# Performance work log

Measured on AMD Instinct MI355X. Metric: run time of the kernel, lower is better.

Reference implementation:

```python
import jax, jax.numpy as jnp
import numpy as np

PAD_IDX = 0
B, T, S, H, V = 64, 32, 64, 1024, 32000


def setup_inputs() -> dict:
    key = jax.random.key(0)
    ks = jax.random.split(key, 12)
    s = 0.02
    emb_tbl = jax.random.normal(ks[0], (V, H), jnp.float32) * s
    emb_tbl = emb_tbl.at[PAD_IDX].set(0.0)  # padding_idx row is zero
    return {
        "input": jax.random.randint(ks[1], (B, T), 0, V),
        "memory": jax.random.normal(ks[2], (1, B, H), jnp.float32),
        "encoder_output": jax.random.normal(ks[3], (B, S, H), jnp.float32),
        "xs_len": jax.random.randint(ks[4], (B,), 1, S + 1),
        "embedding": emb_tbl,
        "w_ih": jax.random.normal(ks[5], (3 * H, 2 * H), jnp.float32) * s,
        "w_hh": jax.random.normal(ks[6], (3 * H, H), jnp.float32) * s,
        "b_ih": jnp.zeros((3 * H,), jnp.float32),
        "b_hh": jnp.zeros((3 * H,), jnp.float32),
        "l1": jax.random.normal(ks[7], (H, H), jnp.float32) * s,
        "l2": jax.random.normal(ks[8], (H, 2 * H), jnp.float32) * s,
        "w_out": jax.random.normal(ks[9], (V, H), jnp.float32) * s,
        "b_out": jnp.zeros((V,), jnp.float32),
    }


def _gru_cell(x, h, w_ih, w_hh, b_ih, b_hh):
    # torch.nn.GRUCell math
    gi = x @ w_ih.T + b_ih          # [B, 3H]
    gh = h @ w_hh.T + b_hh          # [B, 3H]
    ir, iz, inn = jnp.split(gi, 3, axis=1)
    hr, hz, hn = jnp.split(gh, 3, axis=1)
    r = jax.nn.sigmoid(ir + hr)
    z = jax.nn.sigmoid(iz + hz)
    n = jnp.tanh(inn + r * hn)
    return (1.0 - z) * n + z * h


def _attention(hidden, enc, seq_mask, l1, l2):
    # hidden: [B,H], enc: [B,S,H], seq_mask: [B,S] float {0,1}
    q = hidden @ l1.T                              # [B,H]
    score = jnp.einsum("bsh,bh->bs", enc, q)       # [B,S]
    masked = seq_mask * score
    # faithful to `masked_att[masked_att == 0] = -1e10`
    masked = jnp.where(masked == 0.0, -1e10, masked)
    attn = jax.nn.softmax(masked, axis=1)          # softmax over source positions
    ctx = jnp.einsum("bs,bsh->bh", attn, enc)      # [B,H]
    out = jnp.tanh(jnp.concatenate([ctx, hidden], axis=1) @ l2.T)
    return out, attn


def reference(input, memory, encoder_output, xs_len, embedding,
              w_ih, w_hh, b_ih, b_hh, l1, l2, w_out, b_out):
    emb = embedding[input]                         # [B,T,H]
    emb_t = jnp.swapaxes(emb, 0, 1)                # [T,B,H]
    h0 = memory[0]                                 # [B,H]
    ctx0 = jnp.zeros_like(h0)
    s_len = encoder_output.shape[1]
    seq_mask = (jnp.arange(s_len)[None, :] < xs_len[:, None]).astype(emb.dtype)  # [B,S]

    def step(carry, e_t):
        h_prev, ctx = carry
        x = jnp.concatenate([e_t, ctx], axis=1)    # [B,2H]
        h = _gru_cell(x, h_prev, w_ih, w_hh, b_ih, b_hh)
        ctx_new, attn = _attention(h, encoder_output, seq_mask, l1, l2)
        scores = jax.nn.log_softmax(ctx_new @ w_out.T + b_out, axis=1)  # [B,V]
        return (h, ctx_new), (scores, attn)

    (h_fin, ctx_fin), (all_scores, all_attn) = jax.lax.scan(step, (h0, ctx0), emb_t)
    decoder_output = jnp.swapaxes(all_scores, 0, 1)        # [B,T,V]
    decoder_hidden = h_fin[None, :, :]                     # [1,B,H]
    attention_weights = jnp.swapaxes(all_attn, 0, 1)       # [B,T,S]
    return decoder_output, decoder_hidden, attention_weights, ctx_fin
```

## Files before the change

kernel.cpp:

```cpp
#include <hip/hip_runtime.h>


#define B_ 64
#define T_ 32
#define S_ 64
#define H_ 1024
#define V_ 32000
#define NB_ 256
#define LDS_BYTES 152064

#define HID_OFF 65536000L
#define ATT_OFF 65601536L
#define CTF_OFF 65732608L

typedef __attribute__((ext_vector_type(8))) short bf16x8;
typedef __attribute__((ext_vector_type(4))) float f32x4;
typedef __attribute__((ext_vector_type(4))) unsigned int u32x4;
typedef unsigned short u16;
typedef unsigned long long u64;

__device__ __forceinline__ u16 f2bf(float v) {
  unsigned int u = __float_as_uint(v);
  unsigned int r = (u + 0x7fffu + ((u >> 16) & 1u)) >> 16;
  return (u16)r;
}
__device__ __forceinline__ float bf2f(u16 h) {
  return __uint_as_float(((unsigned int)h) << 16);
}
__device__ __forceinline__ void split2(float v, u16* hi, u16* lo) {
  u16 h = f2bf(v);
  *hi = h;
  *lo = f2bf(v - bf2f(h));
}

__device__ __forceinline__ u64 aload_u64(const void* p) {
  return __hip_atomic_load((const u64*)p, __ATOMIC_RELAXED, __HIP_MEMORY_SCOPE_AGENT);
}
__device__ __forceinline__ unsigned aload_u32(const void* p) {
  return __hip_atomic_load((const unsigned*)p, __ATOMIC_RELAXED, __HIP_MEMORY_SCOPE_AGENT);
}
__device__ __forceinline__ void astore_u64(void* p, u64 v) {
  __hip_atomic_store((u64*)p, v, __ATOMIC_RELAXED, __HIP_MEMORY_SCOPE_AGENT);
}
__device__ __forceinline__ void astore_f32(float* p, float v) {
  __hip_atomic_store((unsigned*)p, __float_as_uint(v), __ATOMIC_RELAXED,
                     __HIP_MEMORY_SCOPE_AGENT);
}


__global__ void k_split(const float* __restrict__ src, u16* __restrict__ hi,
                        u16* __restrict__ lo, int n) {
  int i = blockIdx.x * blockDim.x + threadIdx.x;
  int stride = gridDim.x * blockDim.x;
  for (; i < n; i += stride) split2(src[i], &hi[i], &lo[i]);
}

__global__ void k_tobf(const float* __restrict__ src, u16* __restrict__ dst, int n) {
  int i = blockIdx.x * blockDim.x + threadIdx.x;
  int stride = gridDim.x * blockDim.x;
  for (; i < n; i += stride) dst[i] = f2bf(src[i]);
}

__global__ void k_l1t(const float* __restrict__ l1, u16* __restrict__ hi,
                      u16* __restrict__ lo) {
  __shared__ float tile[64][65];
  int it = blockIdx.x & 15, kt = blockIdx.x >> 4;
  for (int q = 0; q < 16; ++q) {
    int idx = q * 256 + threadIdx.x;
    int r = idx >> 6, c = idx & 63;
    tile[r][c] = l1[(long)(it * 64 + r) * H_ + kt * 64 + c];
  }
  __syncthreads();
  for (int q = 0; q < 16; ++q) {
    int idx = q * 256 + threadIdx.x;
    int r = idx >> 6, c = idx & 63;
    long o = (long)(kt * 64 + r) * H_ + it * 64 + c;
    split2(tile[c][r], &hi[o], &lo[o]);
  }
}

__global__ void k_embx(const int* __restrict__ inp, const float* __restrict__ emb,
                       u16* __restrict__ hi, u16* __restrict__ lo) {
  int bt = blockIdx.x;
  int b = bt >> 5, t = bt & 31;
  int id = inp[b * T_ + t];
  const float* src = emb + (long)id * H_;
  long base = (long)(t * B_ + b) * H_;
  for (int k = threadIdx.x; k < H_; k += 256) split2(src[k], &hi[base + k], &lo[base + k]);
}

__global__ void k_h0(const float* __restrict__ mem, u16* __restrict__ hh,
                     u16* __restrict__ hl) {
  int i = blockIdx.x * 256 + threadIdx.x;
  float v = mem[i];
  split2(v, &hh[i], &hl[i]);
}

__global__ void k_guard(float* out, float v) {
  if (blockIdx.x == 0 && threadIdx.x == 0) out[0] = v;
}

template <int SPLIT, int OMODE>
__launch_bounds__(256)
__global__ void k_gemm128(const u16* __restrict__ Ah, const u16* __restrict__ Al,
                          const u16* __restrict__ Bh, const u16* __restrict__ Bl,
                          float* __restrict__ C, const float* __restrict__ bias,
                          int Mtiles, int Ntiles, int K, int Arow, int Brow, int Crow) {
  (void)Ntiles;
  int bx = blockIdx.x;
  int mt = bx % Mtiles, nt = bx / Mtiles;
  int m0 = mt * 128, n0 = nt * 128;

  __shared__ __attribute__((aligned(16))) u16 lds[(SPLIT ? 4 : 2) * 4096];
  char* L = (char*)lds;
  const int tid = threadIdx.x;
  const int lane = tid & 63, wid = tid >> 6;
  const int wm = wid & 1, wn = wid >> 1;
  const int l15 = lane & 15, kq = lane >> 4;

  f32x4 acc[4][4];
  const f32x4 z4 = {0.f, 0.f, 0.f, 0.f};
#pragma unroll
  for (int i = 0; i < 4; ++i)
#pragma unroll
    for (int j = 0; j < 4; ++j) acc[i][j] = z4;

  const int ksteps = K >> 5;
  for (int kt = 0; kt < ksteps; ++kt) {
    __syncthreads();
#pragma unroll
    for (int h2 = 0; h2 < 2; ++h2) {
      int r = (tid >> 2) + (h2 << 6);
      int slot = tid & 3;
      int so = ((slot ^ (r & 3)) << 4);
      long ga = (long)(m0 + r) * Arow + (kt << 5) + (slot << 3);
      long gb = (long)(n0 + r) * Brow + (kt << 5) + (slot << 3);
      *(u32x4*)(L + r * 64 + so) = *(const u32x4*)(Ah + ga);
      *(u32x4*)(L + 8192 + r * 64 + so) = *(const u32x4*)(Bh + gb);
      if (SPLIT) {
        *(u32x4*)(L + 16384 + r * 64 + so) = *(const u32x4*)(Al + ga);
        *(u32x4*)(L + 24576 + r * 64 + so) = *(const u32x4*)(Bl + gb);
      }
    }
    __syncthreads();
    bf16x8 aH[4], bH[4], aL[4], bL[4];
#pragma unroll
    for (int mi = 0; mi < 4; ++mi) {
      int r = (wm << 6) + (mi << 4) + l15;
      int off = r * 64 + ((kq ^ (r & 3)) << 4);
      aH[mi] = *(const bf16x8*)(L + off);
      if (SPLIT) aL[mi] = *(const bf16x8*)(L + 16384 + off);
    }
#pragma unroll
    for (int ni = 0; ni < 4; ++ni) {
      int c = (wn << 6) + (ni << 4) + l15;
      int off = c * 64 + ((kq ^ (c & 3)) << 4);
      bH[ni] = *(const bf16x8*)(L + 8192 + off);
      if (SPLIT) bL[ni] = *(const bf16x8*)(L + 24576 + off);
    }
#pragma unroll
    for (int mi = 0; mi < 4; ++mi)
#pragma unroll
      for (int ni = 0; ni < 4; ++ni) {
        acc[mi][ni] = __builtin_amdgcn_mfma_f32_16x16x32_bf16(aH[mi], bH[ni], acc[mi][ni], 0, 0, 0);
        if (SPLIT) {
          acc[mi][ni] = __builtin_amdgcn_mfma_f32_16x16x32_bf16(aL[mi], bH[ni], acc[mi][ni], 0, 0, 0);
          acc[mi][ni] = __builtin_amdgcn_mfma_f32_16x16x32_bf16(aH[mi], bL[ni], acc[mi][ni], 0, 0, 0);
        }
      }
  }
#pragma unroll
  for (int mi = 0; mi < 4; ++mi)
#pragma unroll
    for (int ni = 0; ni < 4; ++ni)
#pragma unroll
      for (int e = 0; e < 4; ++e) {
        int r = (wm << 6) + (mi << 4) + (kq << 2) + e;
        int c = (wn << 6) + (ni << 4) + l15;
        int gm = m0 + r, gn = n0 + c;
        float v = acc[mi][ni][e];
        if (OMODE == 0) {
          C[(long)gm * Crow + gn] = v;
        } else {
          v += bias[gn];
          C[((long)(gm & 63) * T_ + (gm >> 6)) * V_ + gn] = v;
        }
      }
}

__device__ __forceinline__ void gridbar(unsigned* flags, unsigned seq) {
  __syncthreads();
  if (threadIdx.x == 0)
    __hip_atomic_store(flags + blockIdx.x * 16, seq, __ATOMIC_RELEASE,
                       __HIP_MEMORY_SCOPE_AGENT);
  if (threadIdx.x < 64) {
    int l = threadIdx.x;
    for (;;) {
      unsigned a = __hip_atomic_load(flags + l * 16, __ATOMIC_RELAXED, __HIP_MEMORY_SCOPE_AGENT);
      unsigned b = __hip_atomic_load(flags + (l + 64) * 16, __ATOMIC_RELAXED, __HIP_MEMORY_SCOPE_AGENT);
      unsigned c = __hip_atomic_load(flags + (l + 128) * 16, __ATOMIC_RELAXED, __HIP_MEMORY_SCOPE_AGENT);
      unsigned d = __hip_atomic_load(flags + (l + 192) * 16, __ATOMIC_RELAXED, __HIP_MEMORY_SCOPE_AGENT);
      if (__all((a >= seq) & (b >= seq) & (c >= seq) & (d >= seq))) break;
      __builtin_amdgcn_s_sleep(1);
    }
  }
  __syncthreads();
}

__launch_bounds__(256)
__global__ void k_rec(const float* __restrict__ embi,
                      u16* __restrict__ dctx_h, u16* __restrict__ dctx_l,
                      u16* __restrict__ hh_r, u16* __restrict__ hl_r,
                      const float* __restrict__ memory,
                      const u16* __restrict__ wih_h, const u16* __restrict__ wih_l,
                      const u16* __restrict__ whh_h, const u16* __restrict__ whh_l,
                      const u16* __restrict__ l2_h, const u16* __restrict__ l2_l,
                      float* __restrict__ gip, float* __restrict__ ghp,
                      float* __restrict__ psc, float* __restrict__ ctxp,
                      const float* __restrict__ encT, const float* __restrict__ encL,
                      const int* __restrict__ xs_len,
                      const float* __restrict__ bih, const float* __restrict__ bhh,
                      float* __restrict__ dout, unsigned* flags) {
  extern __shared__ __attribute__((aligned(16))) char L[];
  char* W_HI = L;
  char* W_LO = L + 65536;
  char* A_HI = L + 131072;
  char* A_LO = L + 139264;
  float* hq = (float*)(L + 147456);
  float* at_s = (float*)(L + 148480);
  const int bx = blockIdx.x;
  const int tid = threadIdx.x;
  const int lane = tid & 63, wid = tid >> 6;
  const int wm = wid & 1, wn = wid >> 1;
  const int l15 = lane & 15, kq = lane >> 4;
  const f32x4 z4 = {0.f, 0.f, 0.f, 0.f};
  unsigned seq = 1;

  const int isGI = (bx < 96);
  const int isGH = (bx >= 96 && bx < 192);
  const int isL2 = (bx >= 192 && bx < 224);
  const int sb = bx >> 2;
  const int sq = bx & 3;
  int nt = 0, kc = 0, n0 = 0;
  const u16 *Wg_h = nullptr, *Wg_l = nullptr;
  int wrs = 0;
  if (isGI) {
    nt = bx % 48; kc = bx / 48;
    Wg_h = wih_h + 1024 + (long)nt * 64 * 2048 + kc * 512;
    Wg_l = wih_l + 1024 + (long)nt * 64 * 2048 + kc * 512;
    wrs = 2048;
  } else if (isGH) {
    int j2 = bx - 96;
    nt = j2 % 48; kc = j2 / 48;
    Wg_h = whh_h + (long)nt * 64 * 1024 + kc * 512;
    Wg_l = whh_l + (long)nt * 64 * 1024 + kc * 512;
    wrs = 1024;
  } else if (isL2) {
    n0 = (bx - 192) << 5;
    Wg_h = l2_h + 1024 + (long)n0 * 2048;
    Wg_l = l2_l + 1024 + (long)n0 * 2048;
    wrs = 2048;
  }

  if (isGI || isGH) {
    for (int e = tid; e < 4096; e += 256) {
      int st = e >> 8, r = (e >> 2) & 63, slot = e & 3;
      long g = (long)r * wrs + st * 32 + slot * 8;
      int o = st * 4096 + r * 64 + ((slot ^ (r & 3)) << 4);
      *(u32x4*)(W_HI + o) = *(const u32x4*)(Wg_h + g);
      *(u32x4*)(W_LO + o) = *(const u32x4*)(Wg_l + g);
    }
  } else if (isL2) {
    for (int e = tid; e < 4096; e += 256) {
      int st = e >> 7, r = (e >> 2) & 31, slot = e & 3;
      long g = (long)r * wrs + st * 32 + slot * 8;
      int o = st * 2048 + r * 64 + ((slot ^ (r & 3)) << 4);
      *(u32x4*)(W_HI + o) = *(const u32x4*)(Wg_h + g);
      *(u32x4*)(W_LO + o) = *(const u32x4*)(Wg_l + g);
    }
  }
  __syncthreads();

  float hpv = memory[sb * 1024 + sq * 256 + tid];

  const int pr = tid >> 2, ps = tid & 3;
  const int ao = pr * 64 + ((ps ^ (pr & 3)) << 4);

  for (int t = 0; t < T_; ++t) {
    if (isGI || isGH) {
      const u16* Ah;
      const u16* Al;
      float* outp;
      if (isGI) {
        Ah = dctx_h + (long)t * 65536 + kc * 512;
        Al = dctx_l + (long)t * 65536 + kc * 512;
        outp = gip + (long)kc * 196608 + nt * 64;
      } else {
        Ah = hh_r + (long)t * 65536 + kc * 512;
        Al = hl_r + (long)t * 65536 + kc * 512;
        outp = ghp + (long)kc * 196608 + nt * 64;
      }
      const long g0 = (long)pr * 1024 + ps * 8;
      u32x4 ph0 = *(const u32x4*)(Ah + g0);
      u32x4 ph1 = *(const u32x4*)(Ah + g0 + 32);
      u32x4 pl0 = *(const u32x4*)(Al + g0);
      u32x4 pl1 = *(const u32x4*)(Al + g0 + 32);

      f32x4 acc[2][2];
#pragma unroll
      for (int i = 0; i < 2; ++i)
#pragma unroll
        for (int j = 0; j < 2; ++j) acc[i][j] = z4;

      for (int kt = 0; kt < 8; ++kt) {
        __syncthreads();
        *(u32x4*)(A_HI + ao) = ph0;
        *(u32x4*)(A_HI + 4096 + ao) = ph1;
        *(u32x4*)(A_LO + ao) = pl0;
        *(u32x4*)(A_LO + 4096 + ao) = pl1;
        __syncthreads();
        if (kt < 7) {
          long g = g0 + (kt + 1) * 64;
          ph0 = *(const u32x4*)(Ah + g);
          ph1 = *(const u32x4*)(Ah + g + 32);
          pl0 = *(const u32x4*)(Al + g);
          pl1 = *(const u32x4*)(Al + g + 32);
        }
#pragma unroll
        for (int sub = 0; sub < 2; ++sub) {
          const int stw = (kt * 2 + sub) * 4096;
          const int sta = sub * 4096;
          bf16x8 aH[2], aL[2], bH[2], bL[2];
#pragma unroll
          for (int mi = 0; mi < 2; ++mi) {
            int rr = (wm << 5) + (mi << 4) + l15;
            int off = rr * 64 + ((kq ^ (rr & 3)) << 4);
            aH[mi] = *(const bf16x8*)(A_HI + sta + off);
            aL[mi] = *(const bf16x8*)(A_LO + sta + off);
          }
#pragma unroll
          for (int ni = 0; ni < 2; ++ni) {
            int c = (wn << 5) + (ni << 4) + l15;
            int off = c * 64 + ((kq ^ (c & 3)) << 4);
            bH[ni] = *(const bf16x8*)(W_HI + stw + off);
            bL[ni] = *(const bf16x8*)(W_LO + stw + off);
          }
#pragma unroll
          for (int mi = 0; mi < 2; ++mi)
#pragma unroll
            for (int ni = 0; ni < 2; ++ni) {
              acc[mi][ni] = __builtin_amdgcn_mfma_f32_16x16x32_bf16(aH[mi], bH[ni], acc[mi][ni], 0, 0, 0);
              acc[mi][ni] = __builtin_amdgcn_mfma_f32_16x16x32_bf16(aL[mi], bH[ni], acc[mi][ni], 0, 0, 0);
              acc[mi][ni] = __builtin_amdgcn_mfma_f32_16x16x32_bf16(aH[mi], bL[ni], acc[mi][ni], 0, 0, 0);
            }
        }
      }
#pragma unroll
      for (int mi = 0; mi < 2; ++mi)
#pragma unroll
        for (int ni = 0; ni < 2; ++ni)
#pragma unroll
          for (int e = 0; e < 4; ++e) {
            int r = (wm << 5) + (mi << 4) + (kq << 2) + e;
            int c = (wn << 5) + (ni << 4) + l15;
            astore_f32(outp + (long)r * 3072 + c, acc[mi][ni][e]);
          }
    }
    gridbar(flags, seq++);

    {
      const int b = sb, q = sq;
      const int j = (q << 8) + tid;
      const float* eb = embi + ((long)t * 64 + b) * 3072;
      float g0r = __uint_as_float(aload_u32(gip + b * 3072 + j));
      float g1r = __uint_as_float(aload_u32(gip + 196608 + b * 3072 + j));
      float g0z = __uint_as_float(aload_u32(gip + b * 3072 + 1024 + j));
      float g1z = __uint_as_float(aload_u32(gip + 196608 + b * 3072 + 1024 + j));
      float g0n = __uint_as_float(aload_u32(gip + b * 3072 + 2048 + j));
      float g1n = __uint_as_float(aload_u32(gip + 196608 + b * 3072 + 2048 + j));
      float h0r = __uint_as_float(aload_u32(ghp + b * 3072 + j));
      float h1r = __uint_as_float(aload_u32(ghp + 196608 + b * 3072 + j));
      float h0z = __uint_as_float(aload_u32(ghp + b * 3072 + 1024 + j));
      float h1z = __uint_as_float(aload_u32(ghp + 196608 + b * 3072 + 1024 + j));
      float h0n = __uint_as_float(aload_u32(ghp + b * 3072 + 2048 + j));
      float h1n = __uint_as_float(aload_u32(ghp + 196608 + b * 3072 + 2048 + j));
      float ir = eb[j] + g0r + g1r + bih[j];
      float iz = eb[1024 + j] + g0z + g1z + bih[1024 + j];
      float in2 = eb[2048 + j] + g0n + g1n + bih[2048 + j];
      float hr = h0r + h1r + bhh[j];
      float hz = h0z + h1z + bhh[1024 + j];
      float hn = h0n + h1n + bhh[2048 + j];
      float r = 1.f / (1.f + expf(-(ir + hr)));
      float z = 1.f / (1.f + expf(-(iz + hz)));
      float n = tanhf(in2 + r * hn);
      float h = (1.f - z) * n + z * hpv;
      hpv = h;
      hq[tid] = h;
      if (t == T_ - 1) dout[HID_OFF + (long)b * 1024 + j] = h;
      __syncthreads();
      if (tid < 64) {
        u64 ph = 0, pl = 0;
#pragma unroll
        for (int ii = 0; ii < 4; ++ii) {
          u16 hi, lo;
          split2(hq[tid * 4 + ii], &hi, &lo);
          ph |= (u64)hi << (16 * ii);
          pl |= (u64)lo << (16 * ii);
        }
        long o = (long)(t + 1) * 65536 + (long)b * 1024 + (q << 8) + tid * 4;
        astore_u64(hh_r + o, ph);
        astore_u64(hl_r + o, pl);
      }
      {
        int s = tid >> 2, part = tid & 3;
        const float4* ep = (const float4*)(encT + (((long)b * 64 + s) << 10) + (q << 8) + (part << 6));
        const float4* hp = (const float4*)(hq + (part << 6));
        float dot = 0.f;
#pragma unroll
        for (int kk = 0; kk < 16; ++kk) {
          float4 e = ep[kk], a = hp[kk];
          dot += e.x * a.x + e.y * a.y + e.z * a.z + e.w * a.w;
        }
        dot += __shfl_xor(dot, 1);
        dot += __shfl_xor(dot, 2);
        if (part == 0) astore_f32(psc + (((b << 2) + q) << 6) + s, dot);
      }
    }
    gridbar(flags, seq++);

    {
      const int b = sb, q = sq;
      if (tid < 64) {
        int s = tid;
        float v = 0.f;
#pragma unroll
        for (int qq = 0; qq < 4; ++qq)
          v += __uint_as_float(aload_u32(psc + (((b << 2) + qq) << 6) + s));
        int len = xs_len[b];
        if (s >= len || v == 0.0f) v = -1e10f;
        float m = v;
#pragma unroll
        for (int off = 32; off; off >>= 1) m = fmaxf(m, __shfl_xor(m, off));
        float p = expf(v - m);
        float sum = p;
#pragma unroll
        for (int off = 32; off; off >>= 1) sum += __shfl_xor(sum, off);
        float a = p / sum;
        at_s[s] = a;
        if (q == 0) dout[ATT_OFF + ((long)b * T_ + t) * S_ + s] = a;
      }
      __syncthreads();
      {
        const float* lp = encL + (((long)b * 64 + (q << 4)) << 10) + tid * 4;
        float c0 = 0.f, c1 = 0.f, c2 = 0.f, c3 = 0.f;
#pragma unroll
        for (int s2 = 0; s2 < 16; ++s2) {
          float a = at_s[(q << 4) + s2];
          float4 e = *(const float4*)(lp + (s2 << 10));
          c0 += a * e.x; c1 += a * e.y; c2 += a * e.z; c3 += a * e.w;
        }
        u64 w0 = ((u64)__float_as_uint(c1) << 32) | __float_as_uint(c0);
        u64 w1 = ((u64)__float_as_uint(c3) << 32) | __float_as_uint(c2);
        long o = (((long)(b << 2) + q) << 10) + tid * 4;
        astore_u64(ctxp + o, w0);
        astore_u64(ctxp + o + 2, w1);
      }
    }
    gridbar(flags, seq++);

    if (isL2) {
      const u16* Ah = hh_r + (long)(t + 1) * 65536;
      const u16* Al = hl_r + (long)(t + 1) * 65536;
      const long g0 = (long)pr * 1024 + ps * 8;
      u32x4 ph0 = *(const u32x4*)(Ah + g0);
      u32x4 ph1 = *(const u32x4*)(Ah + g0 + 32);
      u32x4 pl0 = *(const u32x4*)(Al + g0);
      u32x4 pl1 = *(const u32x4*)(Al + g0 + 32);

      f32x4 acc[2];
      acc[0] = z4; acc[1] = z4;
      for (int kt = 0; kt < 16; ++kt) {
        __syncthreads();
        *(u32x4*)(A_HI + ao) = ph0;
        *(u32x4*)(A_HI + 4096 + ao) = ph1;
        *(u32x4*)(A_LO + ao) = pl0;
        *(u32x4*)(A_LO + 4096 + ao) = pl1;
        __syncthreads();
        if (kt < 15) {
          long g = g0 + (kt + 1) * 64;
          ph0 = *(const u32x4*)(Ah + g);
          ph1 = *(const u32x4*)(Ah + g + 32);
          pl0 = *(const u32x4*)(Al + g);
          pl1 = *(const u32x4*)(Al + g + 32);
        }
#pragma unroll
        for (int sub = 0; sub < 2; ++sub) {
          const int stw = (kt * 2 + sub) * 2048;
          const int sta = sub * 4096;
          bf16x8 aH[2], aL[2], bH, bL;
#pragma unroll
          for (int mi = 0; mi < 2; ++mi) {
            int rr = (wm << 5) + (mi << 4) + l15;
            int off = rr * 64 + ((kq ^ (rr & 3)) << 4);
            aH[mi] = *(const bf16x8*)(A_HI + sta + off);
            aL[mi] = *(const bf16x8*)(A_LO + sta + off);
          }
          {
            int c = (wn << 4) + l15;
            int off = c * 64 + ((kq ^ (c & 3)) << 4);
            bH = *(const bf16x8*)(W_HI + stw + off);
            bL = *(const bf16x8*)(W_LO + stw + off);
          }
#pragma unroll
          for (int mi = 0; mi < 2; ++mi) {
            acc[mi] = __builtin_amdgcn_mfma_f32_16x16x32_bf16(aH[mi], bH, acc[mi], 0, 0, 0);
            acc[mi] = __builtin_amdgcn_mfma_f32_16x16x32_bf16(aL[mi], bH, acc[mi], 0, 0, 0);
            acc[mi] = __builtin_amdgcn_mfma_f32_16x16x32_bf16(aH[mi], bL, acc[mi], 0, 0, 0);
          }
        }
      }
      __syncthreads();
      float* cf = (float*)(L + 131072);
#pragma unroll
      for (int mi = 0; mi < 2; ++mi)
#pragma unroll
        for (int e = 0; e < 4; ++e) {
          int rr = (wm << 5) + (mi << 4) + (kq << 2) + e;
          int cc = (wn << 4) + l15;
          float a = 0.f;
#pragma unroll
          for (int qq = 0; qq < 4; ++qq)
            a += __uint_as_float(aload_u32(ctxp + (((long)(rr << 2) + qq) << 10) + n0 + cc));
          float v = tanhf(acc[mi][e] + a);
          if (t == T_ - 1) dout[CTF_OFF + (long)rr * 1024 + n0 + cc] = v;
          cf[rr * 32 + cc] = v;
        }
      __syncthreads();
#pragma unroll
      for (int qq2 = 0; qq2 < 2; ++qq2) {
        int g = tid + qq2 * 256;
        int b = g >> 3, colg = g & 7;
        u64 ph = 0, pl = 0;
#pragma unroll
        for (int ii = 0; ii < 4; ++ii) {
          float v = cf[b * 32 + colg * 4 + ii];
          u16 hi, lo;
          split2(v, &hi, &lo);
          ph |= (u64)hi << (16 * ii);
          pl |= (u64)lo << (16 * ii);
        }
        long o = (long)(t + 1) * 65536 + (long)b * 1024 + n0 + colg * 4;
        astore_u64(dctx_h + o, ph);
        astore_u64(dctx_l + o, pl);
      }
    }
    if (t < T_ - 1) gridbar(flags, seq);
    seq++;
  }
}

__device__ __forceinline__ void lse_comb(float& m, float& s, float mo, float so) {
  float M = fmaxf(m, mo);
  s = s * __expf(m - M) + so * __expf(mo - M);
  m = M;
}

__launch_bounds__(256)
__global__ void k_lsm(float* __restrict__ dout) {
  long base = (long)blockIdx.x * V_;
  int tid = threadIdx.x;
  float m = -3.0e38f, s = 0.f;
  for (int v = tid; v < V_; v += 256) {
    float x = dout[base + v];
    if (x > m) {
      s = s * __expf(m - x) + 1.f;
      m = x;
    } else {
      s += __expf(x - m);
    }
  }
#pragma unroll
  for (int off = 32; off; off >>= 1) {
    float mo = __shfl_xor(m, off), so = __shfl_xor(s, off);
    lse_comb(m, s, mo, so);
  }
  __shared__ float ms[4], ss[4];
  if ((tid & 63) == 0) { ms[tid >> 6] = m; ss[tid >> 6] = s; }
  __syncthreads();
  float M = ms[0], S = ss[0];
  for (int w2 = 1; w2 < 4; ++w2) lse_comb(M, S, ms[w2], ss[w2]);
  float logden = M + logf(S);
  for (int v = tid; v < V_; v += 256) dout[base + v] -= logden;
}

extern "C" void kernel_launch(void* const* d_in, const int* in_sizes, int n_in,
                              void* d_out, int out_size, void* d_ws, size_t ws_size,
                              hipStream_t stream) {
  (void)in_sizes; (void)n_in; (void)out_size;
  const int* input = (const int*)d_in[0];
  const float* memory = (const float*)d_in[1];
  const float* enc = (const float*)d_in[2];
  const int* xs_len = (const int*)d_in[3];
  const float* emb = (const float*)d_in[4];
  const float* wih = (const float*)d_in[5];
  const float* whh = (const float*)d_in[6];
  const float* bih = (const float*)d_in[7];
  const float* bhh = (const float*)d_in[8];
  const float* l1 = (const float*)d_in[9];
  const float* l2 = (const float*)d_in[10];
  const float* wout = (const float*)d_in[11];
  const float* bout = (const float*)d_in[12];
  float* out = (float*)d_out;
  char* w = (char*)d_ws;

  size_t off = 0;
  auto alloc = [&](size_t bytes) {
    size_t o = off;
    off = (off + bytes + 255) & ~(size_t)255;
    return o;
  };
  const size_t N_WIH = 3072UL * 2048, N_WHH = 3072UL * 1024, N_L2 = 1024UL * 2048;
  const size_t N_L1 = 1024UL * 1024, N_ENC = 4096UL * 1024, N_WOUT = 32000UL * 1024;
  const size_t N_EMBX = 2048UL * 1024, N_ENCT = 4096UL * 1024;
  const size_t N_EMBI = 2048UL * 3072, N_ROT = 33UL * 65536;

  size_t o_wih_h = alloc(2 * N_WIH), o_wih_l = alloc(2 * N_WIH);
  size_t o_whh_h = alloc(2 * N_WHH), o_whh_l = alloc(2 * N_WHH);
  size_t o_l2_h = alloc(2 * N_L2), o_l2_l = alloc(2 * N_L2);
  size_t o_l1t_h = alloc(2 * N_L1), o_l1t_l = alloc(2 * N_L1);
  size_t o_ctx_h = alloc(2 * N_ROT), o_ctx_l = alloc(2 * N_ROT);
  size_t o_hh = alloc(2 * N_ROT), o_hl = alloc(2 * N_ROT);
  size_t o_gip = alloc(4 * 2 * 196608), o_ghp = alloc(4 * 2 * 196608);
  size_t o_psc = alloc(4 * 16384);
  size_t o_ctxp = alloc(4 * 262144);
  size_t o_bar = alloc(16384);
  size_t o_arena = alloc(2 * N_ENC * 2 + 2 * N_EMBX * 2 + 4 * N_EMBI + 4 * N_ENCT * 2);

  if (off > ws_size) {
    k_guard<<<1, 1, 0, stream>>>(out, 1.0e8f + (float)(ws_size >> 20));
    return;
  }

  u16* wih_h = (u16*)(w + o_wih_h);   u16* wih_l = (u16*)(w + o_wih_l);
  u16* whh_h = (u16*)(w + o_whh_h);   u16* whh_l = (u16*)(w + o_whh_l);
  u16* l2_h = (u16*)(w + o_l2_h);     u16* l2_l = (u16*)(w + o_l2_l);
  u16* l1t_h = (u16*)(w + o_l1t_h);   u16* l1t_l = (u16*)(w + o_l1t_l);
  u16* ctx_h = (u16*)(w + o_ctx_h);   u16* ctx_l = (u16*)(w + o_ctx_l);
  u16* hh_r = (u16*)(w + o_hh);       u16* hl_r = (u16*)(w + o_hl);
  float* gip = (float*)(w + o_gip);
  float* ghp = (float*)(w + o_ghp);
  float* psc = (float*)(w + o_psc);
  float* ctxp = (float*)(w + o_ctxp);
  unsigned* flags = (unsigned*)(w + o_bar);

  char* ar = w + o_arena;
  u16* enc_h = (u16*)ar;
  u16* enc_l = (u16*)(ar + 2 * N_ENC);
  u16* embx_h = (u16*)(ar + 4 * N_ENC);
  u16* embx_l = (u16*)(ar + 4 * N_ENC + 2 * N_EMBX);
  float* embi = (float*)(ar + 4 * N_ENC + 4 * N_EMBX);
  float* encT = (float*)(ar + 4 * N_ENC + 4 * N_EMBX + 4 * N_EMBI);
  float* encL = (float*)(ar + 4 * N_ENC + 4 * N_EMBX + 4 * N_EMBI + 4 * N_ENCT);
  u16* wout_b = (u16*)ar;

  hipFuncSetAttribute((const void*)k_rec, hipFuncAttributeMaxDynamicSharedMemorySize,
                      LDS_BYTES);

  k_split<<<2048, 256, 0, stream>>>(wih, wih_h, wih_l, (int)N_WIH);
  k_split<<<2048, 256, 0, stream>>>(whh, whh_h, whh_l, (int)N_WHH);
  k_split<<<2048, 256, 0, stream>>>(l2, l2_h, l2_l, (int)N_L2);
  k_split<<<2048, 256, 0, stream>>>(enc, enc_h, enc_l, (int)N_ENC);
  k_l1t<<<256, 256, 0, stream>>>(l1, l1t_h, l1t_l);
  k_embx<<<2048, 256, 0, stream>>>(input, emb, embx_h, embx_l);
  k_h0<<<256, 256, 0, stream>>>(memory, hh_r, hl_r);
  hipMemsetAsync(ctx_h, 0, 131072, stream);
  hipMemsetAsync(ctx_l, 0, 131072, stream);
  hipMemsetAsync(flags, 0, 16384, stream);

  k_gemm128<1, 0><<<256, 256, 0, stream>>>(enc_h, enc_l, l1t_h, l1t_l, encT, nullptr,
                                           32, 8, 1024, 1024, 1024, 1024);
  k_gemm128<1, 0><<<256, 256, 0, stream>>>(enc_h, enc_l, l2_h, l2_l, encL, nullptr,
                                           32, 8, 1024, 1024, 2048, 1024);
  k_gemm128<1, 0><<<384, 256, 0, stream>>>(embx_h, embx_l, wih_h, wih_l, embi, nullptr,
                                           16, 24, 1024, 1024, 2048, 3072);

  k_rec<<<NB_, 256, LDS_BYTES, stream>>>(embi, ctx_h, ctx_l, hh_r, hl_r, memory,
                                         wih_h, wih_l, whh_h, whh_l, l2_h, l2_l,
                                         gip, ghp, psc, ctxp, encT, encL,
                                         xs_len, bih, bhh, out, flags);

  k_tobf<<<4096, 256, 0, stream>>>(wout, wout_b, (int)N_WOUT);

  k_gemm128<0, 1><<<4000, 256, 0, stream>>>(ctx_h + 65536, nullptr, wout_b, nullptr,
                                            out, bout, 16, 250, 1024, 1024, 1024, 0);
  k_lsm<<<2048, 256, 0, stream>>>(out);
}
```

Measured before the change: 2.000 ms.

## Add direct-to-LDS output GEMM, merge split kernels, vectorize log-softmax

Replaces the templated output-projection GEMM with a dedicated kernel that loads tiles with global_load_lds into a swizzled LDS layout and uses an XCD-aware block remap. The four weight/encoder split launches become one fused launch, and the log-softmax kernel now uses float4 loads and stores. The aim is to cut launch overhead, register staging in the large vocabulary GEMM, and scalar memory traffic in the normalization pass. The new GEMM has no double buffering, so load latency is still exposed within each k-step.

```diff
diff --git a/kernel.cpp b/kernel.cpp
--- a/kernel.cpp
+++ b/kernel.cpp
@@ -47,12 +47,30 @@
                      __HIP_MEMORY_SCOPE_AGENT);
 }
 
-
-__global__ void k_split(const float* __restrict__ src, u16* __restrict__ hi,
-                        u16* __restrict__ lo, int n) {
+__device__ __forceinline__ void gll16(const u16* g, u16* l) {
+  __builtin_amdgcn_global_load_lds(
+      (const __attribute__((address_space(1))) void*)g,
+      (__attribute__((address_space(3))) void*)l, 16, 0, 0);
+}
+
+
+__global__ void k_split4(const float* __restrict__ sA, u16* __restrict__ hA,
+                         u16* __restrict__ lA, int nA,
+                         const float* __restrict__ sB, u16* __restrict__ hB,
+                         u16* __restrict__ lB, int nB,
+                         const float* __restrict__ sC, u16* __restrict__ hC,
+                         u16* __restrict__ lC, int nC,
+                         const float* __restrict__ sD, u16* __restrict__ hD,
+                         u16* __restrict__ lD, int nD) {
   int i = blockIdx.x * blockDim.x + threadIdx.x;
   int stride = gridDim.x * blockDim.x;
-  for (; i < n; i += stride) split2(src[i], &hi[i], &lo[i]);
+  int t1 = nA, t2 = nA + nB, t3 = t2 + nC, total = t3 + nD;
+  for (; i < total; i += stride) {
+    if (i < t1) split2(sA[i], &hA[i], &lA[i]);
+    else if (i < t2) { int j = i - t1; split2(sB[j], &hB[j], &lB[j]); }
+    else if (i < t3) { int j = i - t2; split2(sC[j], &hC[j], &lC[j]); }
+    else { int j = i - t3; split2(sD[j], &hD[j], &lD[j]); }
+  }
 }
 
 __global__ void k_tobf(const float* __restrict__ src, u16* __restrict__ dst, int n) {
@@ -100,13 +118,12 @@
   if (blockIdx.x == 0 && threadIdx.x == 0) out[0] = v;
 }
 
-template <int SPLIT, int OMODE>
+template <int SPLIT>
 __launch_bounds__(256)
 __global__ void k_gemm128(const u16* __restrict__ Ah, const u16* __restrict__ Al,
                           const u16* __restrict__ Bh, const u16* __restrict__ Bl,
-                          float* __restrict__ C, const float* __restrict__ bias,
-                          int Mtiles, int Ntiles, int K, int Arow, int Brow, int Crow) {
-  (void)Ntiles;
+                          float* __restrict__ C, int Mtiles, int K, int Arow,
+                          int Brow, int Crow) {
   int bx = blockIdx.x;
   int mt = bx % Mtiles, nt = bx / Mtiles;
   int m0 = mt * 128, n0 = nt * 128;
@@ -177,14 +194,78 @@
       for (int e = 0; e < 4; ++e) {
         int r = (wm << 6) + (mi << 4) + (kq << 2) + e;
         int c = (wn << 6) + (ni << 4) + l15;
+        C[(long)(m0 + r) * Crow + n0 + c] = acc[mi][ni][e];
+      }
+}
+
+__launch_bounds__(256)
+__global__ void k_gemmL(const u16* __restrict__ A, const u16* __restrict__ Bw,
+                        const float* __restrict__ bias, float* __restrict__ C) {
+  int bx = blockIdx.x;
+  int wg = (bx & 7) * 500 + (bx >> 3);
+  int mt = wg & 15, nt = wg >> 4;
+  int m0 = mt << 7, n0 = nt << 7;
+
+  __shared__ __attribute__((aligned(16))) u16 lds[2 * 4096];
+  char* L = (char*)lds;
+  const int tid = threadIdx.x;
+  const int lane = tid & 63, wid = tid >> 6;
+  const int wm = wid & 1, wn = wid >> 1;
+  const int l15 = lane & 15, kq = lane >> 4;
+
+  const int r8 = lane >> 2, ss = lane & 3;
+  const int rA0 = (wid << 4) + r8, rA1 = rA0 + 64;
+  const u16* gA0 = A + (long)(m0 + rA0) * 1024 + ((ss ^ (rA0 & 3)) << 3);
+  const u16* gA1 = A + (long)(m0 + rA1) * 1024 + ((ss ^ (rA1 & 3)) << 3);
+  const u16* gB0 = Bw + (long)(n0 + rA0) * 1024 + ((ss ^ (rA0 & 3)) << 3);
+  const u16* gB1 = Bw + (long)(n0 + rA1) * 1024 + ((ss ^ (rA1 & 3)) << 3);
+  u16* lA0 = (u16*)(L + (wid << 10));
+  u16* lA1 = (u16*)(L + 4096 + (wid << 10));
+  u16* lB0 = (u16*)(L + 8192 + (wid << 10));
+  u16* lB1 = (u16*)(L + 12288 + (wid << 10));
+
+  f32x4 acc[4][4];
+  const f32x4 z4 = {0.f, 0.f, 0.f, 0.f};
+#pragma unroll
+  for (int i = 0; i < 4; ++i)
+#pragma unroll
+    for (int j = 0; j < 4; ++j) acc[i][j] = z4;
+
+  for (int kt = 0; kt < 32; ++kt) {
+    __syncthreads();
+    gll16(gA0 + (kt << 5), lA0);
+    gll16(gA1 + (kt << 5), lA1);
+    gll16(gB0 + (kt << 5), lB0);
+    gll16(gB1 + (kt << 5), lB1);
+    __syncthreads();
+    bf16x8 aF[4], bF[4];
+#pragma unroll
+    for (int mi = 0; mi < 4; ++mi) {
+      int r = (wm << 6) + (mi << 4) + l15;
+      aF[mi] = *(const bf16x8*)(L + r * 64 + ((kq ^ (r & 3)) << 4));
+    }
+#pragma unroll
+    for (int ni = 0; ni < 4; ++ni) {
+      int c = (wn << 6) + (ni << 4) + l15;
+      bF[ni] = *(const bf16x8*)(L + 8192 + c * 64 + ((kq ^ (c & 3)) << 4));
+    }
+#pragma unroll
+    for (int mi = 0; mi < 4; ++mi)
+#pragma unroll
+      for (int ni = 0; ni < 4; ++ni)
+        acc[mi][ni] = __builtin_amdgcn_mfma_f32_16x16x32_bf16(aF[mi], bF[ni], acc[mi][ni], 0, 0, 0);
+  }
+#pragma unroll
+  for (int mi = 0; mi < 4; ++mi)
+#pragma unroll
+    for (int ni = 0; ni < 4; ++ni)
+#pragma unroll
+      for (int e = 0; e < 4; ++e) {
+        int r = (wm << 6) + (mi << 4) + (kq << 2) + e;
+        int c = (wn << 6) + (ni << 4) + l15;
         int gm = m0 + r, gn = n0 + c;
-        float v = acc[mi][ni][e];
-        if (OMODE == 0) {
-          C[(long)gm * Crow + gn] = v;
-        } else {
-          v += bias[gn];
-          C[((long)(gm & 63) * T_ + (gm >> 6)) * V_ + gn] = v;
-        }
+        float v = acc[mi][ni][e] + bias[gn];
+        C[((long)(gm & 63) * T_ + (gm >> 6)) * V_ + gn] = v;
       }
 }
 
@@ -366,7 +447,7 @@
             astore_f32(outp + (long)r * 3072 + c, acc[mi][ni][e]);
           }
     }
-    gridbar(flags, seq++);
+    gridbar(flags, seq); seq++;
 
     {
       const int b = sb, q = sq;
@@ -426,7 +507,7 @@
         if (part == 0) astore_f32(psc + (((b << 2) + q) << 6) + s, dot);
       }
     }
-    gridbar(flags, seq++);
+    gridbar(flags, seq); seq++;
 
     {
       const int b = sb, q = sq;
@@ -466,7 +547,7 @@
         astore_u64(ctxp + o + 2, w1);
       }
     }
-    gridbar(flags, seq++);
+    gridbar(flags, seq); seq++;
 
     if (isL2) {
       const u16* Ah = hh_r + (long)(t + 1) * 65536;
@@ -554,7 +635,7 @@
         astore_u64(dctx_l + o, pl);
       }
     }
-    if (t < T_ - 1) gridbar(flags, seq);
+    if (t < T_ - 1) { gridbar(flags, seq); }
     seq++;
   }
 }
@@ -563,6 +644,14 @@
   float M = fmaxf(m, mo);
   s = s * __expf(m - M) + so * __expf(mo - M);
   m = M;
+}
+__device__ __forceinline__ void lse_push(float& m, float& s, float x) {
+  if (x > m) {
+    s = s * __expf(m - x) + 1.f;
+    m = x;
+  } else {
+    s += __expf(x - m);
+  }
 }
 
 __launch_bounds__(256)
@@ -570,14 +659,17 @@
   long base = (long)blockIdx.x * V_;
   int tid = threadIdx.x;
   float m = -3.0e38f, s = 0.f;
-  for (int v = tid; v < V_; v += 256) {
-    float x = dout[base + v];
-    if (x > m) {
-      s = s * __expf(m - x) + 1.f;
-      m = x;
-    } else {
-      s += __expf(x - m);
-    }
+  const float4* p4 = (const float4*)(dout + base);
+#pragma unroll 4
+  for (int it = 0; it < 31; ++it) {
+    float4 x = p4[it * 256 + tid];
+    lse_push(m, s, x.x); lse_push(m, s, x.y);
+    lse_push(m, s, x.z); lse_push(m, s, x.w);
+  }
+  if (tid < 64) {
+    float4 x = p4[7936 + tid];
+    lse_push(m, s, x.x); lse_push(m, s, x.y);
+    lse_push(m, s, x.z); lse_push(m, s, x.w);
   }
 #pragma unroll
   for (int off = 32; off; off >>= 1) {
@@ -590,7 +682,18 @@
   float M = ms[0], S = ss[0];
   for (int w2 = 1; w2 < 4; ++w2) lse_comb(M, S, ms[w2], ss[w2]);
   float logden = M + logf(S);
-  for (int v = tid; v < V_; v += 256) dout[base + v] -= logden;
+  float4* q4 = (float4*)(dout + base);
+#pragma unroll 4
+  for (int it = 0; it < 31; ++it) {
+    float4 x = q4[it * 256 + tid];
+    x.x -= logden; x.y -= logden; x.z -= logden; x.w -= logden;
+    q4[it * 256 + tid] = x;
+  }
+  if (tid < 64) {
+    float4 x = q4[7936 + tid];
+    x.x -= logden; x.y -= logden; x.z -= logden; x.w -= logden;
+    q4[7936 + tid] = x;
+  }
 }
 
 extern "C" void kernel_launch(void* const* d_in, const int* in_sizes, int n_in,
@@ -666,10 +769,10 @@
   hipFuncSetAttribute((const void*)k_rec, hipFuncAttributeMaxDynamicSharedMemorySize,
                       LDS_BYTES);
 
-  k_split<<<2048, 256, 0, stream>>>(wih, wih_h, wih_l, (int)N_WIH);
-  k_split<<<2048, 256, 0, stream>>>(whh, whh_h, whh_l, (int)N_WHH);
-  k_split<<<2048, 256, 0, stream>>>(l2, l2_h, l2_l, (int)N_L2);
-  k_split<<<2048, 256, 0, stream>>>(enc, enc_h, enc_l, (int)N_ENC);
+  k_split4<<<4096, 256, 0, stream>>>(wih, wih_h, wih_l, (int)N_WIH,
+                                     whh, whh_h, whh_l, (int)N_WHH,
+                                     l2, l2_h, l2_l, (int)N_L2,
+                                     enc, enc_h, enc_l, (int)N_ENC);
   k_l1t<<<256, 256, 0, stream>>>(l1, l1t_h, l1t_l);
   k_embx<<<2048, 256, 0, stream>>>(input, emb, embx_h, embx_l);
   k_h0<<<256, 256, 0, stream>>>(memory, hh_r, hl_r);
@@ -677,12 +780,12 @@
   hipMemsetAsync(ctx_l, 0, 131072, stream);
   hipMemsetAsync(flags, 0, 16384, stream);
 
-  k_gemm128<1, 0><<<256, 256, 0, stream>>>(enc_h, enc_l, l1t_h, l1t_l, encT, nullptr,
-                                           32, 8, 1024, 1024, 1024, 1024);
-  k_gemm128<1, 0><<<256, 256, 0, stream>>>(enc_h, enc_l, l2_h, l2_l, encL, nullptr,
-                                           32, 8, 1024, 1024, 2048, 1024);
-  k_gemm128<1, 0><<<384, 256, 0, stream>>>(embx_h, embx_l, wih_h, wih_l, embi, nullptr,
-                                           16, 24, 1024, 1024, 2048, 3072);
+  k_gemm128<1><<<256, 256, 0, stream>>>(enc_h, enc_l, l1t_h, l1t_l, encT,
+                                        32, 1024, 1024, 1024, 1024);
+  k_gemm128<1><<<256, 256, 0, stream>>>(enc_h, enc_l, l2_h, l2_l, encL,
+                                        32, 1024, 1024, 2048, 1024);
+  k_gemm128<1><<<384, 256, 0, stream>>>(embx_h, embx_l, wih_h, wih_l, embi,
+                                        16, 1024, 1024, 2048, 3072);
 
   k_rec<<<NB_, 256, LDS_BYTES, stream>>>(embi, ctx_h, ctx_l, hh_r, hl_r, memory,
                                          wih_h, wih_l, whh_h, whh_l, l2_h, l2_l,
@@ -691,7 +794,7 @@
 
   k_tobf<<<4096, 256, 0, stream>>>(wout, wout_b, (int)N_WOUT);
 
-  k_gemm128<0, 1><<<4000, 256, 0, stream>>>(ctx_h + 65536, nullptr, wout_b, nullptr,
-                                            out, bout, 16, 250, 1024, 1024, 1024, 0);
+  k_gemmL<<<4000, 256, 0, stream>>>(ctx_h + 65536, wout_b, bout, out);
+
   k_lsm<<<2048, 256, 0, stream>>>(out);
 }
```

New measurement: 1.960 ms. 2.0% less time.
